# Optimization experiments

Hardware: AMD Instinct MI355X
Metric: run time of the kernel (lower is better)

## Reference

```python
import jax, jax.numpy as jnp
import numpy as np

EPS = 1e-4  # Coqui LayerNorm (type '1') eps


def _layer_norm_c(x, g, b):
    # x: (B, C, T); normalize over channel dim 1 (Coqui LayerNorm type '1')
    m = jnp.mean(x, axis=1, keepdims=True)
    v = jnp.var(x, axis=1, keepdims=True)
    return (x - m) * jax.lax.rsqrt(v + EPS) * g[None, :, None] + b[None, :, None]


def _s4d(x, log_dt, A_re, A_im, C_re, C_im, D, Wout, bout):
    # S4 (mode='diag' / S4D) layer, transposed=True -> x: (B, H, L)
    L = x.shape[-1]
    dt = jnp.exp(log_dt)[:, None]                       # (H, 1)
    A = A_re + 1j * A_im                                # (H, N2) diagonal SSM
    dtA = A * dt                                        # (H, N2)
    Cd = (C_re + 1j * C_im) * (jnp.exp(dtA) - 1.0) / A  # ZOH-discretized C (B absorbed)
    vand = jnp.exp(dtA[:, :, None] * jnp.arange(L))     # (H, N2, L) Vandermonde
    K = 2.0 * jnp.einsum('hn,hnl->hl', Cd, vand).real   # (H, L) SSM conv kernel
    n = 2 * L                                           # causal conv via FFT
    y = jnp.fft.irfft(jnp.fft.rfft(x, n=n) * jnp.fft.rfft(K, n=n)[None], n=n)[..., :L]
    y = y + D[None, :, None] * x                        # skip connection
    y = jax.nn.gelu(y, approximate=False)               # dropout=0 (eval)
    z = jnp.einsum('oh,bhl->bol', Wout, y) + bout[None, :, None]  # (B, 2H, L)
    a, g = jnp.split(z, 2, axis=1)                      # GLU over channel dim
    return a * jax.nn.sigmoid(g)


def _ffn(x, x_mask, W1, b1, W2, b2):
    # kernel_size=1 feed-forward conv block with masking
    h = jnp.einsum('fh,bhl->bfl', W1, x * x_mask) + b1[None, :, None]
    h = jax.nn.relu(h)
    o = jnp.einsum('of,bfl->bol', W2, h * x_mask) + b2[None, :, None]
    return o * x_mask


def reference(x, x_mask, log_dt, A_re, A_im, C_re, C_im, D, Wout, bout,
              g1, be1, W1, bf1, W2, bf2, g2, be2):
    n_layers = log_dt.shape[0]
    for i in range(n_layers):
        x = x * x_mask
        y = _s4d(x, log_dt[i], A_re[i], A_im[i], C_re[i], C_im[i],
                 D[i], Wout[i], bout[i])
        x = _layer_norm_c(x + y, g1[i], be1[i])
        y = _ffn(x, x_mask, W1[i], bf1[i], W2[i], bf2[i])
        x = _layer_norm_c(x + y, g2[i], be2[i])
    return x * x_mask


def setup_inputs():
    Lyr, B, H, T, N2, HF = 6, 16, 384, 2048, 32, 1536
    key = jax.random.key(0)
    ks = jax.random.split(key, 8)
    x = jax.random.normal(ks[0], (B, H, T), jnp.float32)
    x_mask = jnp.ones((B, 1, T), jnp.float32)
    # stable S4D init: log_dt in [log 1e-3, log 1e-1], A = -1/2 + i*pi*n
    log_dt = (jax.random.uniform(ks[1], (Lyr, H), jnp.float32)
              * (np.log(0.1) - np.log(0.001)) + np.log(0.001))
    A_re = -0.5 * jnp.ones((Lyr, H, N2), jnp.float32)
    A_im = jnp.broadcast_to(np.pi * jnp.arange(N2, dtype=np.float32),
                            (Lyr, H, N2)) * jnp.ones((1,), jnp.float32)
    C_re = jax.random.normal(ks[2], (Lyr, H, N2), jnp.float32) * 0.5 ** 0.5
    C_im = jax.random.normal(ks[3], (Lyr, H, N2), jnp.float32) * 0.5 ** 0.5
    D = jax.random.normal(ks[4], (Lyr, H), jnp.float32)
    Wout = jax.random.normal(ks[5], (Lyr, 2 * H, H), jnp.float32) / np.sqrt(H)
    bout = jnp.zeros((Lyr, 2 * H), jnp.float32)
    g1 = jnp.ones((Lyr, H), jnp.float32)
    be1 = jnp.zeros((Lyr, H), jnp.float32)
    W1 = jax.random.normal(ks[6], (Lyr, HF, H), jnp.float32) / np.sqrt(H)
    bf1 = jnp.zeros((Lyr, HF), jnp.float32)
    W2 = jax.random.normal(ks[7], (Lyr, H, HF), jnp.float32) / np.sqrt(HF)
    bf2 = jnp.zeros((Lyr, H), jnp.float32)
    g2 = jnp.ones((Lyr, H), jnp.float32)
    be2 = jnp.zeros((Lyr, H), jnp.float32)
    return {"x": x, "x_mask": x_mask, "log_dt": log_dt, "A_re": A_re,
            "A_im": A_im, "C_re": C_re, "C_im": C_im, "D": D,
            "Wout": Wout, "bout": bout, "g1": g1, "be1": be1,
            "W1": W1, "bf1": bf1, "W2": W2, "bf2": bf2,
            "g2": g2, "be2": be2}
```

## Files before the change

kernel.cpp:

```cpp
#include <hip/hip_runtime.h>
#include <math.h>

#define Bq 16
#define Hc 384
#define Tt 2048
#define N2 32
#define LYR 6
#define HFq 1536
#define TWOH 768
#define CHUNK 64
#define NCH (Tt/CHUNK)
#define NJ (Bq*NCH)
#define UH (NJ*CHUNK)

typedef __bf16 bf16x8 __attribute__((ext_vector_type(8)));
typedef float floatx4 __attribute__((ext_vector_type(4)));
typedef _Float16 f16_t;
typedef f16_t fp16x8 __attribute__((ext_vector_type(8)));
typedef f16_t fp16x4 __attribute__((ext_vector_type(4)));

__device__ __forceinline__ unsigned short bfbits(float f) {
  union { float f; unsigned u; } x; x.f = f;
  return (unsigned short)((x.u + 0x7FFF + ((x.u >> 16) & 1)) >> 16);
}
__device__ __forceinline__ float bf2f(unsigned short u) {
  union { unsigned u; float f; } x; x.u = ((unsigned)u) << 16; return x.f;
}

__device__ __forceinline__ void gl_lds16(const void* g, void* l) {
  __builtin_amdgcn_global_load_lds(
      (const __attribute__((address_space(1))) void*)g,
      (__attribute__((address_space(3))) void*)l, 16, 0, 0);
}

__global__ void param_kernel(const float* __restrict__ log_dt,
                             const float* __restrict__ A_re, const float* __restrict__ A_im,
                             const float* __restrict__ C_re, const float* __restrict__ C_im,
                             float* __restrict__ wre, float* __restrict__ wim,
                             float* __restrict__ cdre, float* __restrict__ cdim,
                             float* __restrict__ wSre, float* __restrict__ wSim) {
  int idx = blockIdx.x * blockDim.x + threadIdx.x;
  if (idx >= LYR * Hc * N2) return;
  int hn = idx / N2;
  double dt = exp((double)log_dt[hn]);
  double are = (double)A_re[idx], aim = (double)A_im[idx];
  double dre = are * dt, dimv = aim * dt;
  double er = exp(dre);
  double wr = er * cos(dimv), wi_ = er * sin(dimv);
  double den = are * are + aim * aim;
  double nr = wr - 1.0, ni = wi_;
  double qr = (nr * are + ni * aim) / den;
  double qi = (ni * are - nr * aim) / den;
  double cr = (double)C_re[idx], ci = (double)C_im[idx];
  cdre[idx] = (float)(2.0 * (cr * qr - ci * qi));
  cdim[idx] = (float)(2.0 * (cr * qi + ci * qr));
  wre[idx] = (float)wr; wim[idx] = (float)wi_;
  double es = exp(dre * (double)CHUNK);
  wSre[idx] = (float)(es * cos(dimv * (double)CHUNK));
  wSim[idx] = (float)(es * sin(dimv * (double)CHUNK));
}

__global__ void cvt_bf16_kernel(const float* __restrict__ in, unsigned short* __restrict__ out,
                                int n4) {
  int idx = blockIdx.x * 256 + threadIdx.x;
  if (idx >= n4) return;
  float4 v = ((const float4*)in)[idx];
  ushort4 o;
  o.x = bfbits(v.x); o.y = bfbits(v.y); o.z = bfbits(v.z); o.w = bfbits(v.w);
  ((ushort4*)out)[idx] = o;
}

__global__ __launch_bounds__(256) void transpose_fwd(const float* __restrict__ in,
                                                     float* __restrict__ out) {
  __shared__ float tile[32][33];
  int tx = threadIdx.x, ty = threadIdx.y;
  int t0 = blockIdx.x * 32, c0 = blockIdx.y * 32, b = blockIdx.z;
#pragma unroll
  for (int k = 0; k < 4; k++)
    tile[ty + 8 * k][tx] = in[((size_t)(b * Hc + c0 + ty + 8 * k)) * Tt + t0 + tx];
  __syncthreads();
#pragma unroll
  for (int k = 0; k < 4; k++)
    out[((size_t)(b * Tt + t0 + ty + 8 * k)) * Hc + c0 + tx] = tile[tx][ty + 8 * k];
}

__global__ __launch_bounds__(256) void transpose_bwd(const float* __restrict__ in,
                                                     const float* __restrict__ mask,
                                                     float* __restrict__ out) {
  __shared__ float tile[32][33];
  int tx = threadIdx.x, ty = threadIdx.y;
  int t0 = blockIdx.x * 32, c0 = blockIdx.y * 32, b = blockIdx.z;
#pragma unroll
  for (int k = 0; k < 4; k++)
    tile[ty + 8 * k][tx] = in[((size_t)(b * Tt + t0 + ty + 8 * k)) * Hc + c0 + tx];
  __syncthreads();
  float mv = mask[(size_t)b * Tt + t0 + tx];
#pragma unroll
  for (int k = 0; k < 4; k++)
    out[((size_t)(b * Hc + c0 + ty + 8 * k)) * Tt + t0 + tx] = tile[tx][ty + 8 * k] * mv;
}

__global__ __launch_bounds__(256) void pack_u(const float* __restrict__ xT,
                                              const float* __restrict__ mask,
                                              f16_t* __restrict__ U) {
  __shared__ float tile[64][65];
  int tid = threadIdx.x;
  int t0 = blockIdx.x * 64, h0 = blockIdx.y * 64, b = blockIdx.z;
#pragma unroll
  for (int p = 0; p < 4; p++) {
    int idx = p * 256 + tid;
    int row = idx >> 4, c4 = (idx & 15) * 4;
    float4 v = *(const float4*)&xT[((size_t)(b * Tt + t0 + row)) * Hc + h0 + c4];
    float mv = mask[(size_t)b * Tt + t0 + row];
    tile[row][c4] = v.x * mv; tile[row][c4 + 1] = v.y * mv;
    tile[row][c4 + 2] = v.z * mv; tile[row][c4 + 3] = v.w * mv;
  }
  __syncthreads();
#pragma unroll
  for (int p = 0; p < 2; p++) {
    int idx = p * 256 + tid;
    int hr = idx >> 3, g = (idx & 7) * 8;
    fp16x8 o;
#pragma unroll
    for (int i = 0; i < 8; i++) o[i] = (f16_t)tile[g + i][hr];
    *(fp16x8*)&U[(size_t)(h0 + hr) * UH + (size_t)b * Tt + t0 + g] = o;
  }
}

__global__ __launch_bounds__(256) void build_mats(
    const float* __restrict__ wre, const float* __restrict__ wim,
    const float* __restrict__ cdre, const float* __restrict__ cdim,
    f16_t* __restrict__ Ag, f16_t* __restrict__ Wg) {
  __shared__ float pre[65][32], pim[65][32], Kc[64], cdr_s[32], cdi_s[32];
  int h = blockIdx.x, tid = threadIdx.x;
  if (tid < 32) {
    float wr = wre[h * N2 + tid], wi = wim[h * N2 + tid];
    cdr_s[tid] = cdre[h * N2 + tid];
    cdi_s[tid] = cdim[h * N2 + tid];
    float pr = 1.f, pi = 0.f;
    for (int p = 0; p <= 64; p++) {
      pre[p][tid] = pr; pim[p][tid] = pi;
      float nr2 = pr * wr - pi * wi;
      pi = pr * wi + pi * wr;
      pr = nr2;
    }
  }
  __syncthreads();
  if (tid < 64) {
    float s = 0.f;
    for (int n = 0; n < 32; n++)
      s = fmaf(cdr_s[n], pre[tid][n], fmaf(-cdi_s[n], pim[tid][n], s));
    Kc[tid] = s;
  }
  __syncthreads();
  for (int i = tid; i < 64 * 128; i += 256) {
    int m = i >> 7, k = i & 127;
    float v;
    if (k < 64) {
      v = (m >= k) ? Kc[m - k] : 0.f;
    } else {
      int kk = k - 64, n = kk >> 1;
      v = (kk & 1) ? -fmaf(cdr_s[n], pim[m + 1][n], cdi_s[n] * pre[m + 1][n])
                   :  fmaf(cdr_s[n], pre[m + 1][n], -cdi_s[n] * pim[m + 1][n]);
    }
    Ag[(size_t)h * 8192 + i] = (f16_t)v;
  }
  for (int i = tid; i < 64 * 64; i += 256) {
    int m = i >> 6, tau = i & 63, n = m >> 1;
    float v = (m & 1) ? pim[63 - tau][n] : pre[63 - tau][n];
    Wg[(size_t)h * 4096 + i] = (f16_t)v;
  }
}

__global__ __launch_bounds__(256) void gemm_state(const f16_t* __restrict__ U,
                                                  const f16_t* __restrict__ Wg,
                                                  f16_t* __restrict__ St) {
  __shared__ f16_t Aw[64][72];
  __shared__ f16_t Bu[128][72];
  int tid = threadIdx.x;
  int j0 = blockIdx.x * 128, h = blockIdx.y;
#pragma unroll
  for (int p = 0; p < 2; p++) {
    int idx = p * 256 + tid;
    int row = idx >> 3, c8 = (idx & 7) * 8;
    *(fp16x8*)&Aw[row][c8] = *(const fp16x8*)&Wg[(size_t)h * 4096 + row * 64 + c8];
  }
#pragma unroll
  for (int p = 0; p < 4; p++) {
    int idx = p * 256 + tid;
    int row = idx >> 3, c8 = (idx & 7) * 8;
    *(fp16x8*)&Bu[row][c8] =
        *(const fp16x8*)&U[(size_t)h * UH + (size_t)(j0 + row) * CHUNK + c8];
  }
  __syncthreads();
  int wave = tid >> 6, lane = tid & 63, l16 = lane & 15, quad = lane >> 4;
  int m0 = wave * 16;
  floatx4 acc[8];
#pragma unroll
  for (int jt = 0; jt < 8; jt++) acc[jt] = (floatx4){0.f, 0.f, 0.f, 0.f};
#pragma unroll
  for (int kk = 0; kk < 2; kk++) {
    fp16x8 a = *(const fp16x8*)&Aw[m0 + l16][kk * 32 + quad * 8];
#pragma unroll
    for (int jt = 0; jt < 8; jt++) {
      fp16x8 bb = *(const fp16x8*)&Bu[jt * 16 + l16][kk * 32 + quad * 8];
      acc[jt] = __builtin_amdgcn_mfma_f32_16x16x32_f16(a, bb, acc[jt], 0, 0, 0);
    }
  }
#pragma unroll
  for (int jt = 0; jt < 8; jt++) {
    int j = j0 + jt * 16 + l16;
    fp16x4 o;
#pragma unroll
    for (int r = 0; r < 4; r++) o[r] = (f16_t)acc[jt][r];
    *(fp16x4*)&St[(size_t)h * UH + (size_t)j * CHUNK + m0 + quad * 4] = o;
  }
}

__global__ __launch_bounds__(256) void scan_prefix2(
    f16_t* __restrict__ St,
    const float* __restrict__ wSre, const float* __restrict__ wSim) {
  int gid = blockIdx.x * 256 + threadIdx.x;
  if (gid >= Hc * Bq * N2) return;
  int n = gid & 31;
  int b = (gid >> 5) & 15;
  int h = gid >> 9;
  float wr = wSre[h * N2 + n], wi = wSim[h * N2 + n];
  float cr = 0.f, ci = 0.f;
  unsigned* base = (unsigned*)(St + (size_t)h * UH + (size_t)b * Tt + 2 * n);
  for (int c = 0; c < NCH; c++) {
    union { unsigned u; f16_t h2[2]; } in, out;
    in.u = base[c * 32];
    float sre = (float)in.h2[0], sim = (float)in.h2[1];
    out.h2[0] = (f16_t)cr; out.h2[1] = (f16_t)ci;
    base[c * 32] = out.u;
    float c0 = cr;
    cr = fmaf(wr, c0, fmaf(-wi, ci, sre));
    ci = fmaf(wr, ci, fmaf(wi, c0, sim));
  }
}

__global__ __launch_bounds__(256) void gemm_out(
    const f16_t* __restrict__ U, const f16_t* __restrict__ Ag,
    const f16_t* __restrict__ St, const float* __restrict__ Dv,
    unsigned short* __restrict__ Yb) {
  __shared__ f16_t Aa[64][136];
  __shared__ f16_t Bb[128][136];
  int tid = threadIdx.x;
  int j0 = blockIdx.x * 128, h = blockIdx.y;
#pragma unroll
  for (int p = 0; p < 4; p++) {
    int idx = p * 256 + tid;
    int row = idx >> 4, c8 = (idx & 15) * 8;
    *(fp16x8*)&Aa[row][c8] = *(const fp16x8*)&Ag[(size_t)h * 8192 + row * 128 + c8];
  }
#pragma unroll
  for (int p = 0; p < 4; p++) {
    int idx = p * 256 + tid;
    int row = idx >> 3, c8 = (idx & 7) * 8;
    *(fp16x8*)&Bb[row][c8] =
        *(const fp16x8*)&U[(size_t)h * UH + (size_t)(j0 + row) * CHUNK + c8];
    *(fp16x8*)&Bb[row][64 + c8] =
        *(const fp16x8*)&St[(size_t)h * UH + (size_t)(j0 + row) * CHUNK + c8];
  }
  __syncthreads();
  int wave = tid >> 6, lane = tid & 63, l16 = lane & 15, quad = lane >> 4;
  int m0 = wave * 16;
  floatx4 acc[8];
#pragma unroll
  for (int jt = 0; jt < 8; jt++) acc[jt] = (floatx4){0.f, 0.f, 0.f, 0.f};
#pragma unroll
  for (int kk = 0; kk < 4; kk++) {
    fp16x8 a = *(const fp16x8*)&Aa[m0 + l16][kk * 32 + quad * 8];
#pragma unroll
    for (int jt = 0; jt < 8; jt++) {
      fp16x8 bb = *(const fp16x8*)&Bb[jt * 16 + l16][kk * 32 + quad * 8];
      acc[jt] = __builtin_amdgcn_mfma_f32_16x16x32_f16(a, bb, acc[jt], 0, 0, 0);
    }
  }
  float d = Dv[h];
  int tb = m0 + quad * 4;
#pragma unroll
  for (int jt = 0; jt < 8; jt++) {
    int jr = jt * 16 + l16;
    fp16x4 u4 = *(const fp16x4*)&Bb[jr][tb];
    ushort4 o;
#pragma unroll
    for (int r = 0; r < 4; r++) {
      float v = fmaf(d, (float)u4[r], acc[jt][r]);
      v = 0.5f * v * (1.0f + erff(v * 0.70710678118654752f));
      ((unsigned short*)&o)[r] = bfbits(v);
    }
    *(ushort4*)&Yb[(size_t)h * UH + (size_t)(j0 + jr) * CHUNK + tb] = o;
  }
}

__global__ __launch_bounds__(256) void unpack_y(const unsigned short* __restrict__ Yb,
                                                unsigned short* __restrict__ yb) {
  __shared__ unsigned short tile[64][65];
  int tid = threadIdx.x;
  int t0 = blockIdx.x * 64, h0 = blockIdx.y * 64, b = blockIdx.z;
#pragma unroll
  for (int p = 0; p < 2; p++) {
    int idx = p * 256 + tid;
    int hr = idx >> 3, g = (idx & 7) * 8;
    uint4 v = *(const uint4*)&Yb[(size_t)(h0 + hr) * UH + (size_t)b * Tt + t0 + g];
    const unsigned short* s = (const unsigned short*)&v;
#pragma unroll
    for (int i = 0; i < 8; i++) tile[hr][g + i] = s[i];
  }
  __syncthreads();
#pragma unroll
  for (int p = 0; p < 2; p++) {
    int idx = p * 256 + tid;
    int tr = idx >> 3, g = (idx & 7) * 8;
    unsigned short o[8];
#pragma unroll
    for (int i = 0; i < 8; i++) o[i] = tile[g + i][tr];
    *(uint4*)&yb[((size_t)(b * Tt + t0 + tr)) * Hc + h0 + g] = *(uint4*)o;
  }
}

template <int EPI>
__global__ __launch_bounds__(256) void mfma_gemm(
    const __bf16* __restrict__ act, const __bf16* __restrict__ W,
    const float* __restrict__ bias, const float* __restrict__ mask,
    unsigned short* __restrict__ outb, int K, int NOUT) {
  __shared__ __bf16 As[3][128][32];
  __shared__ __bf16 Bs[3][128][32];
  __shared__ __bf16 Bs2[(EPI == 2) ? 3 : 1][(EPI == 2) ? 128 : 1][32];
  int tid = threadIdx.x;
  int b = blockIdx.z;
  int t0 = blockIdx.x * 128, n0 = blockIdx.y * 128;
  int wave = tid >> 6, lane = tid & 63, l16 = lane & 15, quad = lane >> 4;
  int wm = wave >> 1, wn = wave & 1;

  floatx4 acc[4][4];
  floatx4 accg[(EPI == 2) ? 4 : 1][4];
#pragma unroll
  for (int i = 0; i < 4; i++)
#pragma unroll
    for (int j = 0; j < 4; j++) {
      acc[i][j] = (floatx4){0.f, 0.f, 0.f, 0.f};
      if constexpr (EPI == 2) accg[i][j] = (floatx4){0.f, 0.f, 0.f, 0.f};
    }

  int srow = wave * 16 + (lane >> 2);
  int scol = (((lane & 3) ^ ((lane >> 3) & 3)) * 8);
  const __bf16* aSrc = act + ((size_t)(b * Tt + t0 + srow)) * K + scol;
  const __bf16* bSrc = W + (size_t)(n0 + srow) * K + scol;
  const __bf16* gSrc = W + (size_t)(NOUT + n0 + srow) * K + scol;

  auto stage = [&](int buf, int k0) {
#pragma unroll
    for (int r = 0; r < 2; r++) {
      gl_lds16(aSrc + k0 + (size_t)(64 * r) * K, &As[buf][wave * 16 + r * 64][0]);
      gl_lds16(bSrc + k0 + (size_t)(64 * r) * K, &Bs[buf][wave * 16 + r * 64][0]);
      if constexpr (EPI == 2)
        gl_lds16(gSrc + k0 + (size_t)(64 * r) * K, &Bs2[buf][wave * 16 + r * 64][0]);
    }
  };

  const int NT = K >> 5;
  int swz = (quad ^ ((l16 >> 1) & 3)) << 4;
  stage(0, 0);
  stage(1, 32);
  for (int t = 0; t < NT; ++t) {
    if (t + 1 < NT) {
      asm volatile("s_waitcnt vmcnt(%0)" :: "i"((EPI == 2) ? 6 : 4) : "memory");
    } else {
      asm volatile("s_waitcnt vmcnt(0)" ::: "memory");
    }
    __builtin_amdgcn_s_barrier();
    __builtin_amdgcn_sched_barrier(0);
    int cur = t % 3;
    bf16x8 af[4], bfr[4], gfr[(EPI == 2) ? 4 : 1];
#pragma unroll
    for (int i = 0; i < 4; i++)
      af[i] = *(const bf16x8*)((const char*)&As[cur][0][0] +
                               (wm * 64 + i * 16 + l16) * 64 + swz);
#pragma unroll
    for (int j = 0; j < 4; j++) {
      bfr[j] = *(const bf16x8*)((const char*)&Bs[cur][0][0] +
                                (wn * 64 + j * 16 + l16) * 64 + swz);
      if constexpr (EPI == 2)
        gfr[j] = *(const bf16x8*)((const char*)&Bs2[cur][0][0] +
                                  (wn * 64 + j * 16 + l16) * 64 + swz);
    }
    if (t + 2 < NT) stage((t + 2) % 3, (t + 2) * 32);
#pragma unroll
    for (int i = 0; i < 4; i++)
#pragma unroll
      for (int j = 0; j < 4; j++) {
        acc[i][j] = __builtin_amdgcn_mfma_f32_16x16x32_bf16(af[i], bfr[j], acc[i][j], 0, 0, 0);
        if constexpr (EPI == 2)
          accg[i][j] = __builtin_amdgcn_mfma_f32_16x16x32_bf16(af[i], gfr[j], accg[i][j], 0, 0, 0);
      }
  }

#pragma unroll
  for (int i = 0; i < 4; i++) {
    int tb = t0 + wm * 64 + i * 16 + quad * 4;
    float mv[4];
    if constexpr (EPI == 1) {
#pragma unroll
      for (int r = 0; r < 4; r++) mv[r] = mask[(size_t)b * Tt + tb + r];
    }
#pragma unroll
    for (int j = 0; j < 4; j++) {
      int n = n0 + wn * 64 + j * 16 + l16;
      float bn = bias[n];
      float bg = (EPI == 2) ? bias[NOUT + n] : 0.f;
#pragma unroll
      for (int r = 0; r < 4; r++) {
        size_t o = ((size_t)(b * Tt + tb + r)) * NOUT + n;
        if constexpr (EPI == 0) {
          outb[o] = bfbits(acc[i][j][r] + bn);
        } else if constexpr (EPI == 1) {
          float v = fmaxf(acc[i][j][r] + bn, 0.f) * mv[r];
          outb[o] = bfbits(v);
        } else {
          float a = acc[i][j][r] + bn;
          float g = accg[i][j][r] + bg;
          outb[o] = bfbits(a / (1.f + expf(-g)));
        }
      }
    }
  }
}

__global__ __launch_bounds__(256) void ln_t(
    const float* __restrict__ in1, const unsigned short* __restrict__ in2b,
    const float* __restrict__ mask, const float* __restrict__ gamma,
    const float* __restrict__ beta, float* __restrict__ out,
    unsigned short* __restrict__ outb, int m1, int m2) {
  int row = blockIdx.x * 4 + (threadIdx.x >> 6);
  int lane = threadIdx.x & 63;
  float mv = mask[row];
  float f1 = m1 ? mv : 1.f;
  float f2 = m2 ? mv : 1.f;
  size_t base = (size_t)row * Hc;
  float v[6], sum = 0.f, sq = 0.f;
#pragma unroll
  for (int j = 0; j < 6; j++) {
    int idx = lane + 64 * j;
    float a = in1[base + idx] * f1 + bf2f(in2b[base + idx]) * f2;
    v[j] = a; sum += a; sq = fmaf(a, a, sq);
  }
#pragma unroll
  for (int off = 32; off >= 1; off >>= 1) {
    sum += __shfl_xor(sum, off, 64);
    sq  += __shfl_xor(sq,  off, 64);
  }
  float m = sum * (1.f / Hc);
  float var = sq * (1.f / Hc) - m * m;
  float rs = rsqrtf(var + 1e-4f);
#pragma unroll
  for (int j = 0; j < 6; j++) {
    int idx = lane + 64 * j;
    float o = (v[j] - m) * rs * gamma[idx] + beta[idx];
    out[base + idx] = o;
    if (outb) outb[base + idx] = bfbits(o * mv);
  }
}

__global__ void diag_kernel(float* out, float v) {
  if (blockIdx.x == 0 && threadIdx.x == 0) out[0] = v;
}

extern "C" void kernel_launch(void* const* d_in, const int* in_sizes, int n_in,
                              void* d_out, int out_size, void* d_ws, size_t ws_size,
                              hipStream_t stream) {
  const float* x_in  = (const float*)d_in[0];
  const float* xmask = (const float*)d_in[1];
  const float* log_dt = (const float*)d_in[2];
  const float* A_re = (const float*)d_in[3];
  const float* A_im = (const float*)d_in[4];
  const float* C_re = (const float*)d_in[5];
  const float* C_im = (const float*)d_in[6];
  const float* Dv   = (const float*)d_in[7];
  const float* Wout = (const float*)d_in[8];
  const float* bout = (const float*)d_in[9];
  const float* g1   = (const float*)d_in[10];
  const float* be1  = (const float*)d_in[11];
  const float* W1   = (const float*)d_in[12];
  const float* bf1  = (const float*)d_in[13];
  const float* W2   = (const float*)d_in[14];
  const float* bf2  = (const float*)d_in[15];
  const float* g2   = (const float*)d_in[16];
  const float* be2  = (const float*)d_in[17];

  const size_t NXf   = (size_t)Bq * Hc * Tt;
  const size_t NP    = (size_t)LYR * Hc * N2;
  const size_t YBFf  = NXf / 2;
  const size_t HBFf  = (size_t)Bq * Tt * HFq / 2;
  const size_t WOUTf = (size_t)LYR * TWOH * Hc / 2;
  const size_t W1f   = (size_t)LYR * HFq * Hc / 2;
  const size_t W2f   = (size_t)LYR * Hc * HFq / 2;

  size_t need = 2 * NXf + YBFf + HBFf + WOUTf + W1f + W2f + 6 * NP;
  if (ws_size / 4 < need) {
    diag_kernel<<<1, 64, 0, stream>>>((float*)d_out, 1000.0f + (float)(ws_size >> 20));
    return;
  }

  float* ws = (float*)d_ws;
  float* xT   = ws;
  float* tmp  = xT + NXf;
  float* ybfF = tmp + NXf;
  float* hbfF = ybfF + YBFf;
  float* wobF = hbfF + HBFf;
  float* w1bF = wobF + WOUTf;
  float* w2bF = w1bF + W1f;
  float* wre  = w2bF + W2f;
  float* wim  = wre + NP;
  float* cdre = wim + NP;
  float* cdim = cdre + NP;
  float* wSre = cdim + NP;
  float* wSim = wSre + NP;

  unsigned short* ybf = (unsigned short*)ybfF;
  unsigned short* hbf = (unsigned short*)hbfF;
  unsigned short* wob = (unsigned short*)wobF;
  unsigned short* w1b = (unsigned short*)w1bF;
  unsigned short* w2b = (unsigned short*)w2bF;
  float* x1 = (float*)d_out;

  f16_t* Ub   = (f16_t*)tmp;
  unsigned short* tmpb = (unsigned short*)(tmp + NXf / 2);
  f16_t* St16 = (f16_t*)hbfF;
  unsigned short* Ybi = (unsigned short*)(hbfF + YBFf);
  f16_t* Ag   = (f16_t*)(hbfF + 2 * YBFf);
  f16_t* Wg   = Ag + (size_t)384 * 8192;

  param_kernel<<<(LYR * Hc * N2 + 255) / 256, 256, 0, stream>>>(
      log_dt, A_re, A_im, C_re, C_im, wre, wim, cdre, cdim, wSre, wSim);
  cvt_bf16_kernel<<<(int)(2 * WOUTf + 1023) / 1024, 256, 0, stream>>>(Wout, wob, (int)(WOUTf / 2));
  cvt_bf16_kernel<<<(int)(2 * W1f + 1023) / 1024, 256, 0, stream>>>(W1, w1b, (int)(W1f / 2));
  cvt_bf16_kernel<<<(int)(2 * W2f + 1023) / 1024, 256, 0, stream>>>(W2, w2b, (int)(W2f / 2));
  transpose_fwd<<<dim3(Tt / 32, Hc / 32, Bq), dim3(32, 8), 0, stream>>>(x_in, xT);

  for (int i = 0; i < LYR; i++) {
    size_t po = (size_t)i * Hc * N2;

    pack_u<<<dim3(Tt / 64, Hc / 64, Bq), 256, 0, stream>>>(xT, xmask, Ub);
    build_mats<<<Hc, 256, 0, stream>>>(wre + po, wim + po, cdre + po, cdim + po, Ag, Wg);
    gemm_state<<<dim3(NJ / 128, Hc), 256, 0, stream>>>(Ub, Wg, St16);
    scan_prefix2<<<(Hc * Bq * N2) / 256, 256, 0, stream>>>(St16, wSre + po, wSim + po);
    gemm_out<<<dim3(NJ / 128, Hc), 256, 0, stream>>>(Ub, Ag, St16, Dv + (size_t)i * Hc, Ybi);
    unpack_y<<<dim3(Tt / 64, Hc / 64, Bq), 256, 0, stream>>>(Ybi, ybf);

    mfma_gemm<2><<<dim3(Tt / 128, Hc / 128, Bq), 256, 0, stream>>>(
        (const __bf16*)ybf, (const __bf16*)(wob + (size_t)i * TWOH * Hc),
        bout + (size_t)i * TWOH, xmask, tmpb, Hc, Hc);

    ln_t<<<(Bq * Tt) / 4, 256, 0, stream>>>(
        xT, tmpb, xmask, g1 + (size_t)i * Hc, be1 + (size_t)i * Hc, x1, ybf, 1, 0);

    mfma_gemm<1><<<dim3(Tt / 128, HFq / 128, Bq), 256, 0, stream>>>(
        (const __bf16*)ybf, (const __bf16*)(w1b + (size_t)i * HFq * Hc),
        bf1 + (size_t)i * HFq, xmask, hbf, Hc, HFq);

    mfma_gemm<0><<<dim3(Tt / 128, Hc / 128, Bq), 256, 0, stream>>>(
        (const __bf16*)hbf, (const __bf16*)(w2b + (size_t)i * Hc * HFq),
        bf2 + (size_t)i * Hc, xmask, tmpb, HFq, Hc);

    ln_t<<<(Bq * Tt) / 4, 256, 0, stream>>>(
        x1, tmpb, xmask, g2 + (size_t)i * Hc, be2 + (size_t)i * Hc, xT, nullptr, 0, 1);
  }

  transpose_bwd<<<dim3(Tt / 32, Hc / 32, Bq), dim3(32, 8), 0, stream>>>(xT, xmask, (float*)d_out);
}
```

Baseline: 1.843 ms.

## Fuse state GEMM with chunk prefix scan; enlarge FFN1 GEMM tile to 256 rows

```diff
diff --git a/kernel.cpp b/kernel.cpp
--- a/kernel.cpp
+++ b/kernel.cpp
@@ -172,71 +172,79 @@
   }
 }
 
-__global__ __launch_bounds__(256) void gemm_state(const f16_t* __restrict__ U,
-                                                  const f16_t* __restrict__ Wg,
-                                                  f16_t* __restrict__ St) {
+__global__ __launch_bounds__(512) void gemm_state_prefix(
+    const f16_t* __restrict__ U, const f16_t* __restrict__ Wg,
+    const float* __restrict__ wSre, const float* __restrict__ wSim,
+    f16_t* __restrict__ St) {
   __shared__ f16_t Aw[64][72];
   __shared__ f16_t Bu[128][72];
-  int tid = threadIdx.x;
-  int j0 = blockIdx.x * 128, h = blockIdx.y;
-#pragma unroll
-  for (int p = 0; p < 2; p++) {
-    int idx = p * 256 + tid;
-    int row = idx >> 3, c8 = (idx & 7) * 8;
+  __shared__ f16_t Sl[512][66];
+  int h = blockIdx.x, tid = threadIdx.x;
+  {
+    int row = tid >> 3, c8 = (tid & 7) * 8;
     *(fp16x8*)&Aw[row][c8] = *(const fp16x8*)&Wg[(size_t)h * 4096 + row * 64 + c8];
   }
-#pragma unroll
-  for (int p = 0; p < 4; p++) {
-    int idx = p * 256 + tid;
-    int row = idx >> 3, c8 = (idx & 7) * 8;
-    *(fp16x8*)&Bu[row][c8] =
-        *(const fp16x8*)&U[(size_t)h * UH + (size_t)(j0 + row) * CHUNK + c8];
-  }
-  __syncthreads();
   int wave = tid >> 6, lane = tid & 63, l16 = lane & 15, quad = lane >> 4;
-  int m0 = wave * 16;
-  floatx4 acc[8];
-#pragma unroll
-  for (int jt = 0; jt < 8; jt++) acc[jt] = (floatx4){0.f, 0.f, 0.f, 0.f};
-#pragma unroll
-  for (int kk = 0; kk < 2; kk++) {
-    fp16x8 a = *(const fp16x8*)&Aw[m0 + l16][kk * 32 + quad * 8];
-#pragma unroll
-    for (int jt = 0; jt < 8; jt++) {
-      fp16x8 bb = *(const fp16x8*)&Bu[jt * 16 + l16][kk * 32 + quad * 8];
-      acc[jt] = __builtin_amdgcn_mfma_f32_16x16x32_f16(a, bb, acc[jt], 0, 0, 0);
-    }
-  }
-#pragma unroll
-  for (int jt = 0; jt < 8; jt++) {
-    int j = j0 + jt * 16 + l16;
-    fp16x4 o;
-#pragma unroll
-    for (int r = 0; r < 4; r++) o[r] = (f16_t)acc[jt][r];
-    *(fp16x4*)&St[(size_t)h * UH + (size_t)j * CHUNK + m0 + quad * 4] = o;
-  }
-}
-
-__global__ __launch_bounds__(256) void scan_prefix2(
-    f16_t* __restrict__ St,
-    const float* __restrict__ wSre, const float* __restrict__ wSim) {
-  int gid = blockIdx.x * 256 + threadIdx.x;
-  if (gid >= Hc * Bq * N2) return;
-  int n = gid & 31;
-  int b = (gid >> 5) & 15;
-  int h = gid >> 9;
-  float wr = wSre[h * N2 + n], wi = wSim[h * N2 + n];
-  float cr = 0.f, ci = 0.f;
-  unsigned* base = (unsigned*)(St + (size_t)h * UH + (size_t)b * Tt + 2 * n);
-  for (int c = 0; c < NCH; c++) {
-    union { unsigned u; f16_t h2[2]; } in, out;
-    in.u = base[c * 32];
-    float sre = (float)in.h2[0], sim = (float)in.h2[1];
-    out.h2[0] = (f16_t)cr; out.h2[1] = (f16_t)ci;
-    base[c * 32] = out.u;
-    float c0 = cr;
-    cr = fmaf(wr, c0, fmaf(-wi, ci, sre));
-    ci = fmaf(wr, ci, fmaf(wi, c0, sim));
+  int m0 = (wave & 3) * 16;
+  int jh = wave >> 2;
+  for (int jc = 0; jc < 4; jc++) {
+    __syncthreads();
+#pragma unroll
+    for (int p = 0; p < 2; p++) {
+      int idx = p * 512 + tid;
+      int row = idx >> 3, c8 = (idx & 7) * 8;
+      *(fp16x8*)&Bu[row][c8] =
+          *(const fp16x8*)&U[(size_t)h * UH + (size_t)(jc * 128 + row) * CHUNK + c8];
+    }
+    __syncthreads();
+    floatx4 acc[4];
+#pragma unroll
+    for (int jt = 0; jt < 4; jt++) acc[jt] = (floatx4){0.f, 0.f, 0.f, 0.f};
+#pragma unroll
+    for (int kk = 0; kk < 2; kk++) {
+      fp16x8 a = *(const fp16x8*)&Aw[m0 + l16][kk * 32 + quad * 8];
+#pragma unroll
+      for (int jt = 0; jt < 4; jt++) {
+        fp16x8 bb = *(const fp16x8*)&Bu[jh * 64 + jt * 16 + l16][kk * 32 + quad * 8];
+        acc[jt] = __builtin_amdgcn_mfma_f32_16x16x32_f16(a, bb, acc[jt], 0, 0, 0);
+      }
+    }
+#pragma unroll
+    for (int jt = 0; jt < 4; jt++) {
+      int j = jc * 128 + jh * 64 + jt * 16 + l16;
+      union { unsigned u[2]; f16_t hh[4]; } pk;
+#pragma unroll
+      for (int r = 0; r < 4; r++) pk.hh[r] = (f16_t)acc[jt][r];
+      *(unsigned*)&Sl[j][m0 + quad * 4] = pk.u[0];
+      *(unsigned*)&Sl[j][m0 + quad * 4 + 2] = pk.u[1];
+    }
+  }
+  __syncthreads();
+  {
+    int b = tid >> 5, n = tid & 31;
+    float wr = wSre[h * N2 + n], wi = wSim[h * N2 + n];
+    float cr = 0.f, ci = 0.f;
+    for (int c = 0; c < NCH; c++) {
+      int j = b * NCH + c;
+      union { unsigned u; f16_t hh[2]; } in, out;
+      in.u = *(unsigned*)&Sl[j][2 * n];
+      out.hh[0] = (f16_t)cr; out.hh[1] = (f16_t)ci;
+      *(unsigned*)&Sl[j][2 * n] = out.u;
+      float c0 = cr;
+      cr = fmaf(wr, c0, fmaf(-wi, ci, (float)in.hh[0]));
+      ci = fmaf(wr, ci, fmaf(wi, c0, (float)in.hh[1]));
+    }
+  }
+  __syncthreads();
+  {
+    int j = tid;
+#pragma unroll
+    for (int i = 0; i < 8; i++) {
+      unsigned b4[4];
+#pragma unroll
+      for (int q = 0; q < 4; q++) b4[q] = *(unsigned*)&Sl[j][i * 8 + q * 2];
+      *(uint4*)&St[(size_t)h * UH + (size_t)j * CHUNK + i * 8] = *(uint4*)b4;
+    }
   }
 }
 
@@ -322,16 +330,17 @@
 }
 
 template <int EPI>
-__global__ __launch_bounds__(256) void mfma_gemm(
+__global__ __launch_bounds__((EPI == 1) ? 512 : 256) void mfma_gemm(
     const __bf16* __restrict__ act, const __bf16* __restrict__ W,
     const float* __restrict__ bias, const float* __restrict__ mask,
     unsigned short* __restrict__ outb, int K, int NOUT) {
-  __shared__ __bf16 As[3][128][32];
+  constexpr int BM = (EPI == 1) ? 256 : 128;
+  __shared__ __bf16 As[3][BM][32];
   __shared__ __bf16 Bs[3][128][32];
   __shared__ __bf16 Bs2[(EPI == 2) ? 3 : 1][(EPI == 2) ? 128 : 1][32];
   int tid = threadIdx.x;
   int b = blockIdx.z;
-  int t0 = blockIdx.x * 128, n0 = blockIdx.y * 128;
+  int t0 = blockIdx.x * BM, n0 = blockIdx.y * 128;
   int wave = tid >> 6, lane = tid & 63, l16 = lane & 15, quad = lane >> 4;
   int wm = wave >> 1, wn = wave & 1;
 
@@ -352,14 +361,22 @@
   const __bf16* gSrc = W + (size_t)(NOUT + n0 + srow) * K + scol;
 
   auto stage = [&](int buf, int k0) {
-#pragma unroll
-    for (int r = 0; r < 2; r++) {
-      gl_lds16(aSrc + k0 + (size_t)(64 * r) * K, &As[buf][wave * 16 + r * 64][0]);
-      gl_lds16(bSrc + k0 + (size_t)(64 * r) * K, &Bs[buf][wave * 16 + r * 64][0]);
-      if constexpr (EPI == 2)
-        gl_lds16(gSrc + k0 + (size_t)(64 * r) * K, &Bs2[buf][wave * 16 + r * 64][0]);
+    if constexpr (BM == 256) {
+      gl_lds16(aSrc + k0, &As[buf][wave * 16][0]);
+      gl_lds16(aSrc + k0 + (size_t)128 * K, &As[buf][wave * 16 + 128][0]);
+      gl_lds16(bSrc + k0, &Bs[buf][wave * 16][0]);
+    } else {
+      gl_lds16(aSrc + k0, &As[buf][wave * 16][0]);
+      gl_lds16(aSrc + k0 + (size_t)64 * K, &As[buf][wave * 16 + 64][0]);
+      gl_lds16(bSrc + k0, &Bs[buf][wave * 16][0]);
+      gl_lds16(bSrc + k0 + (size_t)64 * K, &Bs[buf][wave * 16 + 64][0]);
+      if constexpr (EPI == 2) {
+        gl_lds16(gSrc + k0, &Bs2[buf][wave * 16][0]);
+        gl_lds16(gSrc + k0 + (size_t)64 * K, &Bs2[buf][wave * 16 + 64][0]);
+      }
     }
   };
+  constexpr int VC = (EPI == 1) ? 3 : ((EPI == 2) ? 6 : 4);
 
   const int NT = K >> 5;
   int swz = (quad ^ ((l16 >> 1) & 3)) << 4;
@@ -367,7 +384,7 @@
   stage(1, 32);
   for (int t = 0; t < NT; ++t) {
     if (t + 1 < NT) {
-      asm volatile("s_waitcnt vmcnt(%0)" :: "i"((EPI == 2) ? 6 : 4) : "memory");
+      asm volatile("s_waitcnt vmcnt(%0)" :: "i"(VC) : "memory");
     } else {
       asm volatile("s_waitcnt vmcnt(0)" ::: "memory");
     }
@@ -545,8 +562,7 @@
 
     pack_u<<<dim3(Tt / 64, Hc / 64, Bq), 256, 0, stream>>>(xT, xmask, Ub);
     build_mats<<<Hc, 256, 0, stream>>>(wre + po, wim + po, cdre + po, cdim + po, Ag, Wg);
-    gemm_state<<<dim3(NJ / 128, Hc), 256, 0, stream>>>(Ub, Wg, St16);
-    scan_prefix2<<<(Hc * Bq * N2) / 256, 256, 0, stream>>>(St16, wSre + po, wSim + po);
+    gemm_state_prefix<<<Hc, 512, 0, stream>>>(Ub, Wg, wSre + po, wSim + po, St16);
     gemm_out<<<dim3(NJ / 128, Hc), 256, 0, stream>>>(Ub, Ag, St16, Dv + (size_t)i * Hc, Ybi);
     unpack_y<<<dim3(Tt / 64, Hc / 64, Bq), 256, 0, stream>>>(Ybi, ybf);
 
@@ -557,7 +573,7 @@
     ln_t<<<(Bq * Tt) / 4, 256, 0, stream>>>(
         xT, tmpb, xmask, g1 + (size_t)i * Hc, be1 + (size_t)i * Hc, x1, ybf, 1, 0);
 
-    mfma_gemm<1><<<dim3(Tt / 128, HFq / 128, Bq), 256, 0, stream>>>(
+    mfma_gemm<1><<<dim3(Tt / 256, HFq / 128, Bq), 512, 0, stream>>>(
         (const __bf16*)ybf, (const __bf16*)(w1b + (size_t)i * HFq * Hc),
         bf1 + (size_t)i * HFq, xmask, hbf, Hc, HFq);
 
```

Result: no change. 1.840 ms (-0.2%).
